# Kernel tuning notes

Hardware: AMD Instinct MI355X
Metric: run time of the kernel (lower is better)

## Reference

```python
import jax, jax.numpy as jnp
import numpy as np

N = 50000
E = 800000
D_IN = 128
H = 256
L = 3


def setup_inputs() -> dict:
    key = jax.random.key(0)
    ks = jax.random.split(key, 12)
    x = jax.random.normal(ks[0], (N, D_IN), dtype=jnp.float32)
    edge_index = jax.random.randint(ks[1], (2, E), 0, N, dtype=jnp.int32)
    edge_attr = jax.random.uniform(ks[2], (E, 4), dtype=jnp.float32)
    s_enc = 1.0 / np.sqrt(D_IN)
    s_h = 1.0 / np.sqrt(H)
    W_enc = jax.random.uniform(ks[3], (D_IN, H), minval=-s_enc, maxval=s_enc)
    b_enc = jax.random.uniform(ks[4], (H,), minval=-s_enc, maxval=s_enc)
    W_g = jax.random.uniform(ks[5], (L, H, H), minval=-s_h, maxval=s_h)
    b_g = jax.random.uniform(ks[6], (L, H), minval=-s_h, maxval=s_h)
    W_out = jax.random.uniform(ks[7], (H, H), minval=-s_h, maxval=s_h)
    b_out = jax.random.uniform(ks[8], (H,), minval=-s_h, maxval=s_h)
    return {"x": x, "edge_index": edge_index, "edge_attr": edge_attr,
            "W_enc": W_enc, "b_enc": b_enc, "W_g": W_g, "b_g": b_g,
            "W_out": W_out, "b_out": b_out}


def _gcn_norm(edge_index, n):
    # PyG GCNConv: add self-loops, symmetric normalization D^-1/2 (A+I) D^-1/2
    loops = jnp.arange(n, dtype=edge_index.dtype)
    src = jnp.concatenate([edge_index[0], loops])  # [E+N]
    dst = jnp.concatenate([edge_index[1], loops])  # [E+N]
    deg = jax.ops.segment_sum(jnp.ones_like(dst, dtype=jnp.float32), dst, num_segments=n)
    dinv = jnp.where(deg > 0, jax.lax.rsqrt(deg), 0.0)
    norm = dinv[src] * dinv[dst]  # [E+N]
    return src, dst, norm


def _gcn_conv(h, W, b, src, dst, norm, n):
    m = h @ W                                  # [N,H] transform first
    agg = jax.ops.segment_sum(m[src] * norm[:, None], dst, num_segments=n)
    return agg + b


def reference(x, edge_index, edge_attr, W_enc, b_enc, W_g, b_g, W_out, b_out):
    n = x.shape[0]
    src, dst, norm = _gcn_norm(edge_index, n)
    h = jax.nn.relu(x @ W_enc + b_enc)
    for i in range(W_g.shape[0]):
        h = jax.nn.relu(_gcn_conv(h, W_g[i], b_g[i], src, dst, norm, n))
        # dropout is identity in eval mode
    return h @ W_out + b_out
```

## Files before the change

kernel.cpp:

```cpp
#include <hip/hip_runtime.h>
#include <math.h>

#define N_NODES 50000
#define N_EDGES 800000
#define D_IN    128
#define H_DIM   256
#define L_LAYERS 3
#define SCAN_BLOCKS ((N_NODES + 255) / 256)

typedef _Float16 f16x8 __attribute__((ext_vector_type(8)));
typedef _Float16 f16x4 __attribute__((ext_vector_type(4)));
typedef float    f32x4 __attribute__((ext_vector_type(4)));


__global__ __launch_bounds__(256) void hist_kernel(const int* __restrict__ dst,
                                                   int* __restrict__ counts,
                                                   int* __restrict__ rank, int e_cnt) {
    int e = blockIdx.x * 256 + threadIdx.x;
    if (e < e_cnt) rank[e] = atomicAdd(&counts[dst[e]], 1);
}

__global__ __launch_bounds__(256) void scanA_kernel(const int* __restrict__ counts,
                                                    int* __restrict__ blocksum,
                                                    float* __restrict__ dinv, int n) {
    __shared__ int s[256];
    int t = threadIdx.x;
    int i = blockIdx.x * 256 + t;
    int v = (i < n) ? counts[i] : 0;
    if (i < n) dinv[i] = rsqrtf((float)(v + 1));
    s[t] = v;
    __syncthreads();
#pragma unroll
    for (int d = 128; d > 0; d >>= 1) {
        if (t < d) s[t] += s[t + d];
        __syncthreads();
    }
    if (t == 0) blocksum[blockIdx.x] = s[0];
}

__global__ __launch_bounds__(256) void scanB_kernel(int* __restrict__ blocksum,
                                                    int* __restrict__ offsets,
                                                    int nblocks, int n, int total) {
    __shared__ int s[256];
    int t = threadIdx.x;
    int v = (t < nblocks) ? blocksum[t] : 0;
    s[t] = v;
    __syncthreads();
#pragma unroll
    for (int d = 1; d < 256; d <<= 1) {
        int x = (t >= d) ? s[t - d] : 0;
        __syncthreads();
        s[t] += x;
        __syncthreads();
    }
    if (t < nblocks) blocksum[t] = s[t] - v;
    if (t == 0) offsets[n] = total;
}

__global__ __launch_bounds__(256) void scanC_kernel(const int* __restrict__ counts,
                                                    const int* __restrict__ blocksum,
                                                    int* __restrict__ offsets, int n) {
    __shared__ int s[256];
    int t = threadIdx.x;
    int i = blockIdx.x * 256 + t;
    int v = (i < n) ? counts[i] : 0;
    s[t] = v;
    __syncthreads();
#pragma unroll
    for (int d = 1; d < 256; d <<= 1) {
        int x = (t >= d) ? s[t - d] : 0;
        __syncthreads();
        s[t] += x;
        __syncthreads();
    }
    if (i < n) offsets[i] = blocksum[blockIdx.x] + s[t] - v;
}


__global__ __launch_bounds__(256) void fill_kernel(const int* __restrict__ src,
                                                   const int* __restrict__ dst,
                                                   const int* __restrict__ offsets,
                                                   const int* __restrict__ rank,
                                                   const float* __restrict__ dinv,
                                                   int2* __restrict__ csr, int e_cnt) {
    int e = blockIdx.x * 256 + threadIdx.x;
    if (e < e_cnt) {
        int d = dst[e];
        int pos = offsets[d] + rank[e];
        int s = src[e];
        csr[pos] = make_int2(s, __float_as_int(dinv[s]));
    }
}


__global__ __launch_bounds__(256) void aggregate_kernel(const _Float16* __restrict__ h,
                                                        const int* __restrict__ offsets,
                                                        const int2* __restrict__ csr,
                                                        const float* __restrict__ dinv,
                                                        _Float16* __restrict__ outp, int n) {
    int wave = threadIdx.x >> 6;
    int lane = threadIdx.x & 63;
    int v = blockIdx.x * 4 + wave;
    if (v >= n) return;
    int c = lane * 4;
    float dv = dinv[v];
    f16x4 self = *(const f16x4*)(h + (size_t)v * H_DIM + c);
    float ax = dv * (float)self[0];
    float ay = dv * (float)self[1];
    float az = dv * (float)self[2];
    float aw = dv * (float)self[3];

    int e  = offsets[v];
    int e1 = offsets[v + 1];

    for (; e + 15 < e1; e += 16) {
        int2 rec[16]; f16x4 r_[16];
#pragma unroll
        for (int j = 0; j < 16; ++j) rec[j] = csr[e + j];
#pragma unroll
        for (int j = 0; j < 16; ++j) r_[j] = *(const f16x4*)(h + (size_t)rec[j].x * H_DIM + c);
#pragma unroll
        for (int j = 0; j < 16; ++j) {
            float w = __int_as_float(rec[j].y);
            ax += w * (float)r_[j][0];
            ay += w * (float)r_[j][1];
            az += w * (float)r_[j][2];
            aw += w * (float)r_[j][3];
        }
    }
    if (e + 7 < e1) {
        int2 rec[8]; f16x4 r_[8];
#pragma unroll
        for (int j = 0; j < 8; ++j) rec[j] = csr[e + j];
#pragma unroll
        for (int j = 0; j < 8; ++j) r_[j] = *(const f16x4*)(h + (size_t)rec[j].x * H_DIM + c);
#pragma unroll
        for (int j = 0; j < 8; ++j) {
            float w = __int_as_float(rec[j].y);
            ax += w * (float)r_[j][0];
            ay += w * (float)r_[j][1];
            az += w * (float)r_[j][2];
            aw += w * (float)r_[j][3];
        }
        e += 8;
    }
    if (e + 3 < e1) {
        int2 rec[4]; f16x4 r_[4];
#pragma unroll
        for (int j = 0; j < 4; ++j) rec[j] = csr[e + j];
#pragma unroll
        for (int j = 0; j < 4; ++j) r_[j] = *(const f16x4*)(h + (size_t)rec[j].x * H_DIM + c);
#pragma unroll
        for (int j = 0; j < 4; ++j) {
            float w = __int_as_float(rec[j].y);
            ax += w * (float)r_[j][0];
            ay += w * (float)r_[j][1];
            az += w * (float)r_[j][2];
            aw += w * (float)r_[j][3];
        }
        e += 4;
    }
    if (e + 1 < e1) {
        int2 r0 = csr[e], r1 = csr[e + 1];
        f16x4 a = *(const f16x4*)(h + (size_t)r0.x * H_DIM + c);
        f16x4 b = *(const f16x4*)(h + (size_t)r1.x * H_DIM + c);
        float w0 = __int_as_float(r0.y), w1 = __int_as_float(r1.y);
        ax += w0 * (float)a[0] + w1 * (float)b[0];
        ay += w0 * (float)a[1] + w1 * (float)b[1];
        az += w0 * (float)a[2] + w1 * (float)b[2];
        aw += w0 * (float)a[3] + w1 * (float)b[3];
        e += 2;
    }
    if (e < e1) {
        int2 r0 = csr[e];
        f16x4 a = *(const f16x4*)(h + (size_t)r0.x * H_DIM + c);
        float w0 = __int_as_float(r0.y);
        ax += w0 * (float)a[0]; ay += w0 * (float)a[1];
        az += w0 * (float)a[2]; aw += w0 * (float)a[3];
    }
    f16x4 o;
    o[0] = (_Float16)(ax * dv);
    o[1] = (_Float16)(ay * dv);
    o[2] = (_Float16)(az * dv);
    o[3] = (_Float16)(aw * dv);
    *(f16x4*)(outp + (size_t)v * H_DIM + c) = o;
}


#define WCONV_TOTAL 294912

__global__ __launch_bounds__(256) void wconv_kernel(const float* __restrict__ W_enc,
                                                    const float* __restrict__ W_g,
                                                    const float* __restrict__ W_out,
                                                    _Float16* __restrict__ whi,
                                                    _Float16* __restrict__ wlo) {
    int gid = blockIdx.x * 256 + threadIdx.x;
    if (gid >= WCONV_TOTAL) return;
    const float* src; int base, e;
    if (gid < 32768)       { src = W_enc; base = 0;      e = gid; }
    else if (gid < 229376) { src = W_g;   base = 32768;  e = gid - 32768; }
    else                   { src = W_out; base = 229376; e = gid - 229376; }
    int k = e >> 8;
    int n = e & 255;
    float x = src[e];
    _Float16 hb = (_Float16)x;
    _Float16 lb = (_Float16)(x - (float)hb);
    int dst = base + (k >> 5) * 8192 + (n >> 4) * 512 + ((k & 31) >> 3) * 128
            + (n & 15) * 8 + (k & 7);
    whi[dst] = hb;
    wlo[dst] = lb;
}


template <int KC, int AMODE, int OUT16>
__global__ __launch_bounds__(256, 4) void mfma_gemm(const float* __restrict__ Af,
                                                    const _Float16* __restrict__ A16,
                                                    const _Float16* __restrict__ WhG,
                                                    const _Float16* __restrict__ WlG,
                                                    const float* __restrict__ bias,
                                                    float* __restrict__ Cf,
                                                    _Float16* __restrict__ Ch,
                                                    int n, int relu) {
    constexpr int K   = KC * 32;
    constexpr int PKC = (KC >= 8) ? 4 : KC;
    constexpr int NPH = KC / PKC;
    __shared__ _Float16 Wlds[PKC * 2 * 2048];

    int t = threadIdx.x;
    int w = t >> 6;
    int lane = t & 63;
    int q  = blockIdx.x >> 8;
    int rt = blockIdx.x & 255;
    if (rt * 256 >= n) return;
    int colbase = q * 64;
    int mrow = lane & 15;
    int koct = (lane >> 4) * 8;
    int rbase = rt * 256 + w * 64;

    int rows[4];
#pragma unroll
    for (int mt = 0; mt < 4; ++mt) {
        int r = rbase + mt * 16 + mrow;
        rows[mt] = (r < n) ? r : (n - 1);
    }

    f32x4 acc[4][4];
#pragma unroll
    for (int mt = 0; mt < 4; ++mt)
#pragma unroll
        for (int c = 0; c < 4; ++c)
            acc[mt][c] = (f32x4)(0.0f);

    f16x8 a16p[2][4];
    float4 af0[4], af1[4];
    if (AMODE == 1) {
#pragma unroll
        for (int mt = 0; mt < 4; ++mt) {
            a16p[0][mt] = *(const f16x8*)(A16 + (size_t)rows[mt] * K + koct);
            a16p[1][mt] = *(const f16x8*)(A16 + (size_t)rows[mt] * K + 32 + koct);
        }
    } else {
#pragma unroll
        for (int mt = 0; mt < 4; ++mt) {
            const float* p = Af + (size_t)rows[mt] * K + koct;
            af0[mt] = *(const float4*)p;
            af1[mt] = *(const float4*)(p + 4);
        }
    }

#pragma unroll
    for (int ph = 0; ph < NPH; ++ph) {
        if (ph) __syncthreads();
#pragma unroll
        for (int pk = 0; pk < PKC; ++pk) {
            int kc = ph * PKC + pk;
            __builtin_amdgcn_global_load_lds(
                (const __attribute__((address_space(1))) unsigned int*)(WhG + (size_t)kc * 8192 + q * 2048 + t * 8),
                (__attribute__((address_space(3))) unsigned int*)(&Wlds[(pk * 2 + 0) * 2048 + t * 8]), 16, 0, 0);
            __builtin_amdgcn_global_load_lds(
                (const __attribute__((address_space(1))) unsigned int*)(WlG + (size_t)kc * 8192 + q * 2048 + t * 8),
                (__attribute__((address_space(3))) unsigned int*)(&Wlds[(pk * 2 + 1) * 2048 + t * 8]), 16, 0, 0);
        }
        __syncthreads();

#pragma unroll
        for (int pk = 0; pk < PKC; ++pk) {
            int kc = ph * PKC + pk;
            f16x8 ah[4], al[4];
            if (AMODE == 0) {
#pragma unroll
                for (int mt = 0; mt < 4; ++mt) {
                    float4 c0 = af0[mt], c1 = af1[mt];
                    if (kc + 1 < KC) {
                        const float* p = Af + (size_t)rows[mt] * K + (kc + 1) * 32 + koct;
                        af0[mt] = *(const float4*)p;
                        af1[mt] = *(const float4*)(p + 4);
                    }
                    float xs[8] = {c0.x, c0.y, c0.z, c0.w, c1.x, c1.y, c1.z, c1.w};
                    f16x8 H, L;
#pragma unroll
                    for (int j = 0; j < 8; ++j) {
                        _Float16 hb = (_Float16)xs[j];
                        H[j] = hb;
                        L[j] = (_Float16)(xs[j] - (float)hb);
                    }
                    ah[mt] = H;
                    al[mt] = L;
                }
            }

#pragma unroll
            for (int c = 0; c < 4; ++c) {
                f16x8 bh = *(const f16x8*)&Wlds[(pk * 2 + 0) * 2048 + c * 512 + lane * 8];
                f16x8 bl = *(const f16x8*)&Wlds[(pk * 2 + 1) * 2048 + c * 512 + lane * 8];
#pragma unroll
                for (int mt = 0; mt < 4; ++mt) {
                    if (AMODE == 1) {
                        f16x8 a = a16p[kc & 1][mt];
                        acc[mt][c] = __builtin_amdgcn_mfma_f32_16x16x32_f16(a, bh, acc[mt][c], 0, 0, 0);
                        acc[mt][c] = __builtin_amdgcn_mfma_f32_16x16x32_f16(a, bl, acc[mt][c], 0, 0, 0);
                    } else {
                        acc[mt][c] = __builtin_amdgcn_mfma_f32_16x16x32_f16(ah[mt], bh, acc[mt][c], 0, 0, 0);
                        acc[mt][c] = __builtin_amdgcn_mfma_f32_16x16x32_f16(ah[mt], bl, acc[mt][c], 0, 0, 0);
                        acc[mt][c] = __builtin_amdgcn_mfma_f32_16x16x32_f16(al[mt], bh, acc[mt][c], 0, 0, 0);
                    }
                }
            }

            if (AMODE == 1 && kc + 2 < KC) {
#pragma unroll
                for (int mt = 0; mt < 4; ++mt)
                    a16p[kc & 1][mt] = *(const f16x8*)(A16 + (size_t)rows[mt] * K + (kc + 2) * 32 + koct);
            }
        }
    }

    int colq = lane & 15;
    int rowq = (lane >> 4) * 4;
#pragma unroll
    for (int c = 0; c < 4; ++c) {
        int col = colbase + c * 16 + colq;
        float b = bias[col];
#pragma unroll
        for (int mt = 0; mt < 4; ++mt) {
            int rb = rbase + mt * 16 + rowq;
#pragma unroll
            for (int r = 0; r < 4; ++r) {
                int row = rb + r;
                if (row < n) {
                    float v = acc[mt][c][r] + b;
                    if (relu) v = fmaxf(v, 0.f);
                    if (OUT16) Ch[(size_t)row * H_DIM + col] = (_Float16)v;
                    else       Cf[(size_t)row * H_DIM + col] = v;
                }
            }
        }
    }
}


extern "C" void kernel_launch(void* const* d_in, const int* in_sizes, int n_in,
                              void* d_out, int out_size, void* d_ws, size_t ws_size,
                              hipStream_t stream) {
    const float* x     = (const float*)d_in[0];
    const int*   ei    = (const int*)d_in[1];
    const float* W_enc = (const float*)d_in[3];
    const float* b_enc = (const float*)d_in[4];
    const float* W_g   = (const float*)d_in[5];
    const float* b_g   = (const float*)d_in[6];
    const float* W_out = (const float*)d_in[7];
    const float* b_out = (const float*)d_in[8];
    float* out = (float*)d_out;

    char* ws = (char*)d_ws;
    size_t off = 0;
    auto alloc = [&](size_t bytes) -> void* {
        void* p = ws + off;
        off = (off + bytes + 255) & ~(size_t)255;
        return p;
    };
    int*       counts   = (int*)alloc((size_t)N_NODES * 4);
    int*       offsets  = (int*)alloc((size_t)(N_NODES + 1) * 4);
    float*     dinv     = (float*)alloc((size_t)N_NODES * 4);
    int*       blocksum = (int*)alloc((size_t)SCAN_BLOCKS * 4);
    int*       rank     = (int*)alloc((size_t)N_EDGES * 4);
    int2*      csr      = (int2*)alloc((size_t)N_EDGES * 8);
    _Float16*  h16      = (_Float16*)alloc((size_t)N_NODES * H_DIM * 2);
    _Float16*  agg16    = (_Float16*)alloc((size_t)N_NODES * H_DIM * 2);
    _Float16*  whi      = (_Float16*)alloc((size_t)WCONV_TOTAL * 2);
    _Float16*  wlo      = (_Float16*)alloc((size_t)WCONV_TOTAL * 2);

    const int* src = ei;
    const int* dst = ei + N_EDGES;

    hipMemsetAsync(counts, 0, (size_t)N_NODES * 4, stream);
    hist_kernel<<<(N_EDGES + 255) / 256, 256, 0, stream>>>(dst, counts, rank, N_EDGES);
    scanA_kernel<<<SCAN_BLOCKS, 256, 0, stream>>>(counts, blocksum, dinv, N_NODES);
    scanB_kernel<<<1, 256, 0, stream>>>(blocksum, offsets, SCAN_BLOCKS, N_NODES, N_EDGES);
    scanC_kernel<<<SCAN_BLOCKS, 256, 0, stream>>>(counts, blocksum, offsets, N_NODES);
    fill_kernel<<<(N_EDGES + 255) / 256, 256, 0, stream>>>(src, dst, offsets, rank, dinv,
                                                           csr, N_EDGES);
    wconv_kernel<<<(WCONV_TOTAL + 255) / 256, 256, 0, stream>>>(W_enc, W_g, W_out, whi, wlo);

    mfma_gemm<4, 0, 1><<<1024, 256, 0, stream>>>(x, (const _Float16*)nullptr,
                                                 whi, wlo, b_enc,
                                                 (float*)nullptr, h16, N_NODES, 1);
    for (int l = 0; l < L_LAYERS; ++l) {
        aggregate_kernel<<<N_NODES / 4, 256, 0, stream>>>(h16, offsets, csr, dinv,
                                                          agg16, N_NODES);
        mfma_gemm<8, 1, 1><<<1024, 256, 0, stream>>>((const float*)nullptr, agg16,
                                                     whi + 32768 + (size_t)l * 65536,
                                                     wlo + 32768 + (size_t)l * 65536,
                                                     b_g + (size_t)l * H_DIM,
                                                     (float*)nullptr, h16, N_NODES, 1);
    }
    mfma_gemm<8, 1, 0><<<1024, 256, 0, stream>>>((const float*)nullptr, h16,
                                                 whi + 229376, wlo + 229376, b_out,
                                                 out, (_Float16*)nullptr, N_NODES, 0);
}
```

Before: 492.5 us.

## Fuse neighbor aggregation with layer GEMM via LDS tile per 16 nodes

Replaces the separate aggregate kernel and per-layer MFMA GEMM with one fused kernel. Each block aggregates 16 nodes into an LDS tile, then multiplies that tile by the layer weight using MFMA (hi+lo fp16 split) and writes the ReLU output to a ping-pong buffer. This drops the intermediate aggregate write/read and one launch per layer. In exchange every block reloads the full 256x256 weight pair from global/L2, each wave serially aggregates 4 nodes, and the GEMM runs on small 16-row tiles with lower MFMA efficiency.

```diff
diff --git a/kernel.cpp b/kernel.cpp
--- a/kernel.cpp
+++ b/kernel.cpp
@@ -7,6 +7,7 @@
 #define H_DIM   256
 #define L_LAYERS 3
 #define SCAN_BLOCKS ((N_NODES + 255) / 256)
+#define FUSED_BLOCKS (N_NODES / 16)
 
 typedef _Float16 f16x8 __attribute__((ext_vector_type(8)));
 typedef _Float16 f16x4 __attribute__((ext_vector_type(4)));
@@ -75,7 +76,6 @@
     }
     if (i < n) offsets[i] = blocksum[blockIdx.x] + s[t] - v;
 }
-
 
 __global__ __launch_bounds__(256) void fill_kernel(const int* __restrict__ src,
                                                    const int* __restrict__ dst,
@@ -93,97 +93,140 @@
 }
 
 
-__global__ __launch_bounds__(256) void aggregate_kernel(const _Float16* __restrict__ h,
-                                                        const int* __restrict__ offsets,
-                                                        const int2* __restrict__ csr,
-                                                        const float* __restrict__ dinv,
-                                                        _Float16* __restrict__ outp, int n) {
+__global__ __launch_bounds__(256) void fused_layer(const _Float16* __restrict__ h_in,
+                                                   const int* __restrict__ offsets,
+                                                   const int2* __restrict__ csr,
+                                                   const float* __restrict__ dinv,
+                                                   const _Float16* __restrict__ WhL,
+                                                   const _Float16* __restrict__ WlL,
+                                                   const float* __restrict__ bias,
+                                                   _Float16* __restrict__ h_out) {
+    __shared__ _Float16 Alds[16][264];
     int wave = threadIdx.x >> 6;
     int lane = threadIdx.x & 63;
-    int v = blockIdx.x * 4 + wave;
-    if (v >= n) return;
+    int nb = blockIdx.x * 16;
     int c = lane * 4;
-    float dv = dinv[v];
-    f16x4 self = *(const f16x4*)(h + (size_t)v * H_DIM + c);
-    float ax = dv * (float)self[0];
-    float ay = dv * (float)self[1];
-    float az = dv * (float)self[2];
-    float aw = dv * (float)self[3];
-
-    int e  = offsets[v];
-    int e1 = offsets[v + 1];
-
-    for (; e + 15 < e1; e += 16) {
-        int2 rec[16]; f16x4 r_[16];
-#pragma unroll
-        for (int j = 0; j < 16; ++j) rec[j] = csr[e + j];
-#pragma unroll
-        for (int j = 0; j < 16; ++j) r_[j] = *(const f16x4*)(h + (size_t)rec[j].x * H_DIM + c);
-#pragma unroll
-        for (int j = 0; j < 16; ++j) {
-            float w = __int_as_float(rec[j].y);
-            ax += w * (float)r_[j][0];
-            ay += w * (float)r_[j][1];
-            az += w * (float)r_[j][2];
-            aw += w * (float)r_[j][3];
-        }
-    }
-    if (e + 7 < e1) {
-        int2 rec[8]; f16x4 r_[8];
-#pragma unroll
-        for (int j = 0; j < 8; ++j) rec[j] = csr[e + j];
-#pragma unroll
-        for (int j = 0; j < 8; ++j) r_[j] = *(const f16x4*)(h + (size_t)rec[j].x * H_DIM + c);
-#pragma unroll
-        for (int j = 0; j < 8; ++j) {
-            float w = __int_as_float(rec[j].y);
-            ax += w * (float)r_[j][0];
-            ay += w * (float)r_[j][1];
-            az += w * (float)r_[j][2];
-            aw += w * (float)r_[j][3];
-        }
-        e += 8;
-    }
-    if (e + 3 < e1) {
-        int2 rec[4]; f16x4 r_[4];
-#pragma unroll
-        for (int j = 0; j < 4; ++j) rec[j] = csr[e + j];
-#pragma unroll
-        for (int j = 0; j < 4; ++j) r_[j] = *(const f16x4*)(h + (size_t)rec[j].x * H_DIM + c);
-#pragma unroll
-        for (int j = 0; j < 4; ++j) {
-            float w = __int_as_float(rec[j].y);
-            ax += w * (float)r_[j][0];
-            ay += w * (float)r_[j][1];
-            az += w * (float)r_[j][2];
-            aw += w * (float)r_[j][3];
-        }
-        e += 4;
-    }
-    if (e + 1 < e1) {
-        int2 r0 = csr[e], r1 = csr[e + 1];
-        f16x4 a = *(const f16x4*)(h + (size_t)r0.x * H_DIM + c);
-        f16x4 b = *(const f16x4*)(h + (size_t)r1.x * H_DIM + c);
-        float w0 = __int_as_float(r0.y), w1 = __int_as_float(r1.y);
-        ax += w0 * (float)a[0] + w1 * (float)b[0];
-        ay += w0 * (float)a[1] + w1 * (float)b[1];
-        az += w0 * (float)a[2] + w1 * (float)b[2];
-        aw += w0 * (float)a[3] + w1 * (float)b[3];
-        e += 2;
-    }
-    if (e < e1) {
-        int2 r0 = csr[e];
-        f16x4 a = *(const f16x4*)(h + (size_t)r0.x * H_DIM + c);
-        float w0 = __int_as_float(r0.y);
-        ax += w0 * (float)a[0]; ay += w0 * (float)a[1];
-        az += w0 * (float)a[2]; aw += w0 * (float)a[3];
-    }
-    f16x4 o;
-    o[0] = (_Float16)(ax * dv);
-    o[1] = (_Float16)(ay * dv);
-    o[2] = (_Float16)(az * dv);
-    o[3] = (_Float16)(aw * dv);
-    *(f16x4*)(outp + (size_t)v * H_DIM + c) = o;
+
+    for (int i = 0; i < 4; ++i) {
+        int v = nb + 4 * wave + i;
+        float dv = dinv[v];
+        f16x4 self = *(const f16x4*)(h_in + (size_t)v * H_DIM + c);
+        float ax = dv * (float)self[0];
+        float ay = dv * (float)self[1];
+        float az = dv * (float)self[2];
+        float aw = dv * (float)self[3];
+
+        int e  = offsets[v];
+        int e1 = offsets[v + 1];
+
+        for (; e + 15 < e1; e += 16) {
+            int2 rec[16]; f16x4 r_[16];
+#pragma unroll
+            for (int j = 0; j < 16; ++j) rec[j] = csr[e + j];
+#pragma unroll
+            for (int j = 0; j < 16; ++j) r_[j] = *(const f16x4*)(h_in + (size_t)rec[j].x * H_DIM + c);
+#pragma unroll
+            for (int j = 0; j < 16; ++j) {
+                float w = __int_as_float(rec[j].y);
+                ax += w * (float)r_[j][0];
+                ay += w * (float)r_[j][1];
+                az += w * (float)r_[j][2];
+                aw += w * (float)r_[j][3];
+            }
+        }
+        if (e + 7 < e1) {
+            int2 rec[8]; f16x4 r_[8];
+#pragma unroll
+            for (int j = 0; j < 8; ++j) rec[j] = csr[e + j];
+#pragma unroll
+            for (int j = 0; j < 8; ++j) r_[j] = *(const f16x4*)(h_in + (size_t)rec[j].x * H_DIM + c);
+#pragma unroll
+            for (int j = 0; j < 8; ++j) {
+                float w = __int_as_float(rec[j].y);
+                ax += w * (float)r_[j][0];
+                ay += w * (float)r_[j][1];
+                az += w * (float)r_[j][2];
+                aw += w * (float)r_[j][3];
+            }
+            e += 8;
+        }
+        if (e + 3 < e1) {
+            int2 rec[4]; f16x4 r_[4];
+#pragma unroll
+            for (int j = 0; j < 4; ++j) rec[j] = csr[e + j];
+#pragma unroll
+            for (int j = 0; j < 4; ++j) r_[j] = *(const f16x4*)(h_in + (size_t)rec[j].x * H_DIM + c);
+#pragma unroll
+            for (int j = 0; j < 4; ++j) {
+                float w = __int_as_float(rec[j].y);
+                ax += w * (float)r_[j][0];
+                ay += w * (float)r_[j][1];
+                az += w * (float)r_[j][2];
+                aw += w * (float)r_[j][3];
+            }
+            e += 4;
+        }
+        if (e + 1 < e1) {
+            int2 r0 = csr[e], r1 = csr[e + 1];
+            f16x4 a = *(const f16x4*)(h_in + (size_t)r0.x * H_DIM + c);
+            f16x4 b = *(const f16x4*)(h_in + (size_t)r1.x * H_DIM + c);
+            float w0 = __int_as_float(r0.y), w1 = __int_as_float(r1.y);
+            ax += w0 * (float)a[0] + w1 * (float)b[0];
+            ay += w0 * (float)a[1] + w1 * (float)b[1];
+            az += w0 * (float)a[2] + w1 * (float)b[2];
+            aw += w0 * (float)a[3] + w1 * (float)b[3];
+            e += 2;
+        }
+        if (e < e1) {
+            int2 r0 = csr[e];
+            f16x4 a = *(const f16x4*)(h_in + (size_t)r0.x * H_DIM + c);
+            float w0 = __int_as_float(r0.y);
+            ax += w0 * (float)a[0]; ay += w0 * (float)a[1];
+            az += w0 * (float)a[2]; aw += w0 * (float)a[3];
+        }
+        f16x4 o;
+        o[0] = (_Float16)(ax * dv);
+        o[1] = (_Float16)(ay * dv);
+        o[2] = (_Float16)(az * dv);
+        o[3] = (_Float16)(aw * dv);
+        *(f16x4*)&Alds[4 * wave + i][c] = o;
+    }
+    __syncthreads();
+
+    int mrow = lane & 15;
+    int g    = lane >> 4;
+    const _Float16* Wh = WhL + (size_t)wave * 2048 + (size_t)lane * 8;
+    const _Float16* Wl = WlL + (size_t)wave * 2048 + (size_t)lane * 8;
+
+    f32x4 acc2[4];
+#pragma unroll
+    for (int cc = 0; cc < 4; ++cc) acc2[cc] = (f32x4)(0.0f);
+
+#pragma unroll
+    for (int kc = 0; kc < 8; ++kc) {
+        f16x8 a = *(const f16x8*)&Alds[mrow][kc * 32 + g * 8];
+#pragma unroll
+        for (int cc = 0; cc < 4; ++cc) {
+            f16x8 bh = *(const f16x8*)(Wh + kc * 8192 + cc * 512);
+            f16x8 bl = *(const f16x8*)(Wl + kc * 8192 + cc * 512);
+            acc2[cc] = __builtin_amdgcn_mfma_f32_16x16x32_f16(a, bh, acc2[cc], 0, 0, 0);
+            acc2[cc] = __builtin_amdgcn_mfma_f32_16x16x32_f16(a, bl, acc2[cc], 0, 0, 0);
+        }
+    }
+
+    int colq = lane & 15;
+    int rowq = g * 4;
+#pragma unroll
+    for (int cc = 0; cc < 4; ++cc) {
+        int col = wave * 64 + cc * 16 + colq;
+        float b = bias[col];
+#pragma unroll
+        for (int r = 0; r < 4; ++r) {
+            float vv = acc2[cc][r] + b;
+            vv = fmaxf(vv, 0.f);
+            h_out[(size_t)(nb + rowq + r) * H_DIM + col] = (_Float16)vv;
+        }
+    }
 }
 
 
@@ -386,7 +429,7 @@
     int*       rank     = (int*)alloc((size_t)N_EDGES * 4);
     int2*      csr      = (int2*)alloc((size_t)N_EDGES * 8);
     _Float16*  h16      = (_Float16*)alloc((size_t)N_NODES * H_DIM * 2);
-    _Float16*  agg16    = (_Float16*)alloc((size_t)N_NODES * H_DIM * 2);
+    _Float16*  hbuf     = (_Float16*)alloc((size_t)N_NODES * H_DIM * 2);
     _Float16*  whi      = (_Float16*)alloc((size_t)WCONV_TOTAL * 2);
     _Float16*  wlo      = (_Float16*)alloc((size_t)WCONV_TOTAL * 2);
 
@@ -405,16 +448,17 @@
     mfma_gemm<4, 0, 1><<<1024, 256, 0, stream>>>(x, (const _Float16*)nullptr,
                                                  whi, wlo, b_enc,
                                                  (float*)nullptr, h16, N_NODES, 1);
+    _Float16* ping = h16;
+    _Float16* pong = hbuf;
     for (int l = 0; l < L_LAYERS; ++l) {
-        aggregate_kernel<<<N_NODES / 4, 256, 0, stream>>>(h16, offsets, csr, dinv,
-                                                          agg16, N_NODES);
-        mfma_gemm<8, 1, 1><<<1024, 256, 0, stream>>>((const float*)nullptr, agg16,
-                                                     whi + 32768 + (size_t)l * 65536,
-                                                     wlo + 32768 + (size_t)l * 65536,
-                                                     b_g + (size_t)l * H_DIM,
-                                                     (float*)nullptr, h16, N_NODES, 1);
-    }
-    mfma_gemm<8, 1, 0><<<1024, 256, 0, stream>>>((const float*)nullptr, h16,
+        fused_layer<<<FUSED_BLOCKS, 256, 0, stream>>>(ping, offsets, csr, dinv,
+                                                      whi + 32768 + (size_t)l * 65536,
+                                                      wlo + 32768 + (size_t)l * 65536,
+                                                      b_g + (size_t)l * H_DIM,
+                                                      pong);
+        _Float16* tmp = ping; ping = pong; pong = tmp;
+    }
+    mfma_gemm<8, 1, 0><<<1024, 256, 0, stream>>>((const float*)nullptr, ping,
                                                  whi + 229376, wlo + 229376, b_out,
                                                  out, (_Float16*)nullptr, N_NODES, 0);
 }
```

Result: no change. 498.2 us (+1.1%).
